# Kernel tuning notes

Measured on AMD Instinct MI355X. Metric: run time of the kernel, lower is better.

## Reference

```python
import jax, jax.numpy as jnp
import numpy as np

B, S, E, H = 2, 2048, 1024, 16
D = E // H  # head_dim = 64
SCALE = D ** -0.5
NEG = -1e9


def setup_inputs() -> dict:
    key = jax.random.key(0)
    ks = jax.random.split(key, 10)
    hidden_states = jax.random.normal(ks[0], (B, S, E), dtype=jnp.float32)
    # CLIP-style additive causal mask [B, 1, L, S]
    causal = jnp.where(jnp.tril(jnp.ones((S, S), dtype=bool)), 0.0, NEG).astype(jnp.float32)
    attn_mask = jnp.broadcast_to(causal, (B, 1, S, S))
    def lin(kw, kb):
        W = jax.random.normal(kw, (E, E), dtype=jnp.float32) * (E ** -0.5)
        b = jax.random.normal(kb, (E,), dtype=jnp.float32) * 0.02
        return W, b
    Wq, bq = lin(ks[1], ks[2])
    Wk, bk = lin(ks[3], ks[4])
    Wv, bv = lin(ks[5], ks[6])
    Wo, bo = lin(ks[7], ks[8])
    return {"hidden_states": hidden_states, "attn_mask": attn_mask,
            "Wq": Wq, "bq": bq, "Wk": Wk, "bk": bk,
            "Wv": Wv, "bv": bv, "Wo": Wo, "bo": bo}


def reference(hidden_states, attn_mask, Wq, bq, Wk, bk, Wv, bv, Wo, bo):
    b, L, e = hidden_states.shape
    # projections (nn.Linear: x @ W.T + b)
    def split_heads(x):
        return x.reshape(b, L, H, D).transpose(0, 2, 1, 3)  # [b,h,l,d]
    q = split_heads(hidden_states @ Wq.T + bq)
    k = split_heads(hidden_states @ Wk.T + bk)
    v = split_heads(hidden_states @ Wv.T + bv)
    # QK^T * scale + additive mask, softmax, AV (dropout_p = 0 in eval)
    scores = jnp.einsum('bhld,bhsd->bhls', q, k) * SCALE + attn_mask
    attn = jax.nn.softmax(scores, axis=-1)
    ctx = jnp.einsum('bhls,bhsd->bhld', attn, v)
    ctx = ctx.transpose(0, 2, 1, 3).reshape(b, L, e)
    return ctx @ Wo.T + bo
```

## Files before the change

kernel.cpp:

```cpp
#include <hip/hip_runtime.h>
#include <hip/hip_bf16.h>
#include <stdint.h>


typedef __hip_bfloat16 bf16;
typedef short bf16x8 __attribute__((ext_vector_type(8)));
typedef short bf16x4 __attribute__((ext_vector_type(4)));
typedef float f32x4 __attribute__((ext_vector_type(4)));

__device__ __forceinline__ f32x4 mfma16(bf16x8 a, bf16x8 b, f32x4 c) {
  return __builtin_amdgcn_mfma_f32_16x16x32_bf16(a, b, c, 0, 0, 0);
}

__device__ __forceinline__ f32x4 mfma_k16(bf16x4 a, bf16x4 b, f32x4 c) {
#if __has_builtin(__builtin_amdgcn_mfma_f32_16x16x16bf16_1k)
  return __builtin_amdgcn_mfma_f32_16x16x16bf16_1k(a, b, c, 0, 0, 0);
#else
  f32x4 d;
  asm volatile("v_mfma_f32_16x16x16_bf16 %0, %1, %2, %3\n\ts_nop 7\n\ts_nop 7"
               : "=v"(d)
               : "v"(a), "v"(b), "v"(c));
  return d;
#endif
}

__device__ __forceinline__ void async16(const void* g, void* l) {
  __builtin_amdgcn_global_load_lds((const __attribute__((address_space(1))) void*)g,
                                   (__attribute__((address_space(3))) void*)l, 16, 0, 0);
}

__global__ __launch_bounds__(256) void cvt_kernel(
    const float* __restrict__ hs, const float* __restrict__ Wq,
    const float* __restrict__ Wk, const float* __restrict__ Wv,
    const float* __restrict__ Wo, bf16* __restrict__ dst) {
  const size_t e = ((size_t)blockIdx.x * 256 + threadIdx.x) * 8;
  const float* src;
  size_t off;
  if (e < 4194304) {
    src = hs; off = e;
  } else {
    const size_t w = e - 4194304;
    const int wi = (int)(w >> 20);
    src = (wi == 0) ? Wq : (wi == 1) ? Wk : (wi == 2) ? Wv : Wo;
    off = w & 1048575;
  }
  const float4 a = *(const float4*)(src + off);
  const float4 b = *(const float4*)(src + off + 4);
  union { bf16 h[8]; uint4 u; } p;
  p.h[0] = __float2bfloat16(a.x); p.h[1] = __float2bfloat16(a.y);
  p.h[2] = __float2bfloat16(a.z); p.h[3] = __float2bfloat16(a.w);
  p.h[4] = __float2bfloat16(b.x); p.h[5] = __float2bfloat16(b.y);
  p.h[6] = __float2bfloat16(b.z); p.h[7] = __float2bfloat16(b.w);
  *(uint4*)(dst + e) = p.u;
}

__global__ __launch_bounds__(256, 3) void qkv_gemm(
    const bf16* __restrict__ X, const bf16* __restrict__ Wb,
    const float* __restrict__ bq, const float* __restrict__ bk,
    const float* __restrict__ bv, bf16* __restrict__ out) {
  constexpr int Kd = 1024;
  __shared__ bf16 sA[2][128 * 32];
  __shared__ bf16 sB[2][128 * 32];
  const int tid = threadIdx.x;
  const int wave = tid >> 6, lane = tid & 63;
  const int g = lane >> 4, ln = lane & 15;
  const int tM = blockIdx.y * 128, tN = blockIdx.x * 128;
  const int which = tN >> 10;
  const bf16* W = Wb + (size_t)which * 1048576;
  const float* bias = (which == 0) ? bq : (which == 1) ? bk : bv;
  const int tNl = tN & 1023;
  const float oscale = (which == 0) ? 0.18033688011112042f : 1.0f;
  const int wrow = (wave >> 1) * 64, wcol = (wave & 1) * 64;
  const f32x4 fz = {0.f, 0.f, 0.f, 0.f};

  f32x4 acc[4][4];
#pragma unroll
  for (int i = 0; i < 4; ++i)
#pragma unroll
    for (int j = 0; j < 4; ++j) acc[i][j] = fz;

  int srow[4], scol[4];
#pragma unroll
  for (int t = 0; t < 4; ++t) {
    const int d = tid + t * 256;
    srow[t] = (d >> 2) & 127;
    scol[t] = ((d >> 9) << 5) + ((d & 3) << 3);
  }

  for (int k0 = 0; k0 < Kd; k0 += 64) {
    __syncthreads();
#pragma unroll
    for (int t = 0; t < 4; ++t) {
      const int d = tid + t * 256;
      async16(X + (size_t)(tM + srow[t]) * Kd + k0 + scol[t], &sA[0][0] + d * 8);
      async16(W + (size_t)(tNl + srow[t]) * Kd + k0 + scol[t], &sB[0][0] + d * 8);
    }
    __syncthreads();
#pragma unroll
    for (int kk = 0; kk < 2; ++kk) {
      bf16x8 aF[4], bF[4];
#pragma unroll
      for (int i = 0; i < 4; ++i)
        aF[i] = *(const bf16x8*)(&sA[kk][0] + (wrow + i * 16 + ln) * 32 + g * 8);
#pragma unroll
      for (int j = 0; j < 4; ++j)
        bF[j] = *(const bf16x8*)(&sB[kk][0] + (wcol + j * 16 + ln) * 32 + g * 8);
#pragma unroll
      for (int i = 0; i < 4; ++i)
#pragma unroll
        for (int j = 0; j < 4; ++j) acc[i][j] = mfma16(aF[i], bF[j], acc[i][j]);
    }
  }

  bf16* outw = out + (size_t)which * 4194304;
#pragma unroll
  for (int j = 0; j < 4; ++j) {
    const int nl = tNl + wcol + j * 16 + ln;
    const float bvf = bias[nl];
    const int h = nl >> 6, d = nl & 63;
#pragma unroll
    for (int i = 0; i < 4; ++i) {
#pragma unroll
      for (int r = 0; r < 4; ++r) {
        const int m = tM + wrow + i * 16 + g * 4 + r;
        const int b = m >> 11, s = m & 2047;
        const float v = (acc[i][j][r] + bvf) * oscale;
        outw[(((size_t)(b * 16 + h) * 2048 + s) << 6) + d] = __float2bfloat16(v);
      }
    }
  }
}

__global__ __launch_bounds__(256, 4) void out_gemm(
    const bf16* __restrict__ X, const bf16* __restrict__ W,
    const float* __restrict__ bias, float* __restrict__ out) {
  constexpr int Kd = 1024;
  __shared__ bf16 sA[64 * 32];
  __shared__ bf16 sB[64 * 32];
  const int tid = threadIdx.x;
  const int wave = tid >> 6, lane = tid & 63;
  const int g = lane >> 4, ln = lane & 15;
  const int tM = blockIdx.y * 64, tN = blockIdx.x * 64;
  const f32x4 fz = {0.f, 0.f, 0.f, 0.f};

  f32x4 acc[4];
#pragma unroll
  for (int j = 0; j < 4; ++j) acc[j] = fz;

  const int srow = tid >> 2, scol = (tid & 3) << 3;
  for (int k0 = 0; k0 < Kd; k0 += 32) {
    __syncthreads();
    async16(X + (size_t)(tM + srow) * Kd + k0 + scol, sA + tid * 8);
    async16(W + (size_t)(tN + srow) * Kd + k0 + scol, sB + tid * 8);
    __syncthreads();
    const bf16x8 aF = *(const bf16x8*)(sA + (wave * 16 + ln) * 32 + g * 8);
    bf16x8 bF[4];
#pragma unroll
    for (int j = 0; j < 4; ++j)
      bF[j] = *(const bf16x8*)(sB + (j * 16 + ln) * 32 + g * 8);
#pragma unroll
    for (int j = 0; j < 4; ++j) acc[j] = mfma16(aF, bF[j], acc[j]);
  }

#pragma unroll
  for (int j = 0; j < 4; ++j) {
    const int n = tN + j * 16 + ln;
    const float bvf = bias[n];
#pragma unroll
    for (int r = 0; r < 4; ++r) {
      const int m = tM + wave * 16 + g * 4 + r;
      out[(size_t)m * 1024 + n] = acc[j][r] + bvf;
    }
  }
}

__global__ __launch_bounds__(256, 4) void attn_kernel(
    const bf16* __restrict__ Q, const bf16* __restrict__ K,
    const bf16* __restrict__ V, bf16* __restrict__ O) {
  constexpr int S = 2048, D = 64;
  __shared__ bf16 sK[64 * 72];
  __shared__ bf16 sVf[64 * 64];

  const int tid = threadIdx.x;
  const int w = tid >> 6, lane = tid & 63;
  const int g = lane >> 4, ln = lane & 15;
  const int px = blockIdx.x, py = blockIdx.y;
  const int bh = (px & 7) * 4 + (py & 3);
  const int qidx = (px >> 3) + 4 * (py >> 2);
  const int qt = 31 - qidx;
  const int b = bh >> 4, h = bh & 15;
  const f32x4 fz = {0.f, 0.f, 0.f, 0.f};

  const bf16* Qb = Q + (size_t)bh * S * D;
  const bf16* Kb = K + (size_t)bh * S * D;
  const bf16* Vb = V + (size_t)bh * S * D;

  const int kr0 = tid >> 3, kc0 = (tid & 7) << 3;
  int vsrc[2][4], vdst[2];
#pragma unroll
  for (int t = 0; t < 2; ++t) {
    const int c = tid + t * 256;
    const int u = c * 2;
    const int kbdb = u >> 6, vg = (u >> 4) & 3, l0 = u & 15;
    const int kb = kbdb >> 2, db = kbdb & 3;
#pragma unroll
    for (int i = 0; i < 4; ++i) vsrc[t][i] = (kb * 16 + vg * 4 + i) * 64 + db * 16 + l0;
    vdst[t] = c * 8;
  }

  bf16x8 qf[2];
#pragma unroll
  for (int kc = 0; kc < 2; ++kc)
    qf[kc] = *(const bf16x8*)(Qb + (size_t)(qt * 64 + w * 16 + ln) * D + kc * 32 + g * 8);

  f32x4 oacc[4];
#pragma unroll
  for (int db = 0; db < 4; ++db) oacc[db] = fz;
  f32x4 lacc = fz;
  const short onebf = (short)0x3F80;
  const bf16x4 onesf = {onebf, onebf, onebf, onebf};

  uint4 kreg0 = *(const uint4*)(Kb + (size_t)kr0 * D + kc0);
  uint4 kreg1 = *(const uint4*)(Kb + (size_t)(kr0 + 32) * D + kc0);
  uint32_t vreg[2][4];
#pragma unroll
  for (int t = 0; t < 2; ++t)
#pragma unroll
    for (int i = 0; i < 4; ++i) vreg[t][i] = *(const uint32_t*)(Vb + vsrc[t][i]);

  for (int kt = 0; kt <= qt; ++kt) {
    __syncthreads();
    *(uint4*)(sK + kr0 * 72 + kc0) = kreg0;
    *(uint4*)(sK + (kr0 + 32) * 72 + kc0) = kreg1;
#pragma unroll
    for (int t = 0; t < 2; ++t) {
      const uint32_t d0 = vreg[t][0], d1 = vreg[t][1], d2 = vreg[t][2], d3 = vreg[t][3];
      uint4 pk;
      pk.x = (d1 << 16) | (d0 & 0xffffu);
      pk.y = (d3 << 16) | (d2 & 0xffffu);
      pk.z = (d1 & 0xffff0000u) | (d0 >> 16);
      pk.w = (d3 & 0xffff0000u) | (d2 >> 16);
      *(uint4*)(sVf + vdst[t]) = pk;
    }
    __syncthreads();
    if (kt < qt) {
      const size_t nb = (size_t)(kt + 1) * 64;
      kreg0 = *(const uint4*)(Kb + (nb + kr0) * D + kc0);
      kreg1 = *(const uint4*)(Kb + (nb + kr0 + 32) * D + kc0);
#pragma unroll
      for (int t = 0; t < 2; ++t)
#pragma unroll
        for (int i = 0; i < 4; ++i)
          vreg[t][i] = *(const uint32_t*)(Vb + nb * D + vsrc[t][i]);
    }

    f32x4 sacc[4];
#pragma unroll
    for (int kb = 0; kb < 4; ++kb) sacc[kb] = fz;
#pragma unroll
    for (int kb = 0; kb < 4; ++kb) {
      const bf16x8 k0 = *(const bf16x8*)(sK + (kb * 16 + ln) * 72 + g * 8);
      const bf16x8 k1 = *(const bf16x8*)(sK + (kb * 16 + ln) * 72 + 32 + g * 8);
      sacc[kb] = mfma16(k0, qf[0], sacc[kb]);
      sacc[kb] = mfma16(k1, qf[1], sacc[kb]);
    }

    const bool diag = (kt == qt);
    const int qloc = w * 16 + ln;
    bf16x4 pa[4];
#pragma unroll
    for (int kb = 0; kb < 4; ++kb) {
      union { bf16 hh[4]; bf16x4 v; } pu;
#pragma unroll
      for (int r = 0; r < 4; ++r) {
        float pv = exp2f(sacc[kb][r]);
        if (diag && (kb * 16 + g * 4 + r > qloc)) pv = 0.f;
        pu.hh[r] = __float2bfloat16(pv);
      }
      pa[kb] = pu.v;
      lacc = mfma_k16(pa[kb], onesf, lacc);
    }

#pragma unroll
    for (int db = 0; db < 4; ++db) {
#pragma unroll
      for (int kb = 0; kb < 4; ++kb) {
        const bf16x4 vf =
            *(const bf16x4*)(sVf + ((kb * 4 + db) * 64 + g * 16 + ln) * 4);
        oacc[db] = mfma_k16(pa[kb], vf, oacc[db]);
      }
    }
  }

  float invl[4];
#pragma unroll
  for (int r = 0; r < 4; ++r) invl[r] = 1.0f / lacc[r];

#pragma unroll
  for (int db = 0; db < 4; ++db)
#pragma unroll
    for (int r = 0; r < 4; ++r) {
      const int row = qt * 64 + w * 16 + g * 4 + r;
      const int col = db * 16 + ln;
      O[(((size_t)(b * 2048 + row) * 16 + h) << 6) + col] =
          __float2bfloat16(oacc[db][r] * invl[r]);
    }
}

extern "C" void kernel_launch(void* const* d_in, const int* in_sizes, int n_in,
                              void* d_out, int out_size, void* d_ws, size_t ws_size,
                              hipStream_t stream) {
  const float* hs = (const float*)d_in[0];
  const float* Wq = (const float*)d_in[2];
  const float* bq = (const float*)d_in[3];
  const float* Wk = (const float*)d_in[4];
  const float* bk = (const float*)d_in[5];
  const float* Wv = (const float*)d_in[6];
  const float* bv = (const float*)d_in[7];
  const float* Wo = (const float*)d_in[8];
  const float* bo = (const float*)d_in[9];
  float* out = (float*)d_out;

  char* ws = (char*)d_ws;
  bf16* XW = (bf16*)ws;
  bf16* Xb = XW;
  bf16* W3b = XW + 4194304;
  bf16* Wob = XW + 7340032;
  bf16* Qw = (bf16*)(ws + (16u << 20));
  bf16* Kw = (bf16*)(ws + (24u << 20));
  bf16* Vw = (bf16*)(ws + (32u << 20));
  bf16* Cw = (bf16*)ws;

  const dim3 blk(256);
  cvt_kernel<<<4096, blk, 0, stream>>>(hs, Wq, Wk, Wv, Wo, XW);
  qkv_gemm<<<dim3(24, 32), blk, 0, stream>>>(Xb, W3b, bq, bk, bv, Qw);
  attn_kernel<<<dim3(32, 32), blk, 0, stream>>>(Qw, Kw, Vw, Cw);
  out_gemm<<<dim3(16, 64), blk, 0, stream>>>(Cw, Wob, bo, out);
}
```

Measured before the change: 200.7 us.

## Process 128 query rows per attention block with 512 threads sharing K/V tiles

The attention kernel now uses 512-thread blocks covering 128 query rows (8 waves), with half as many blocks. Each K/V tile staged in shared memory is reused by twice as many waves, and each thread loads one K row-chunk and one V chunk instead of two. Waves whose query rows lie entirely before the current key tile skip compute but still take part in the barriers. This adds idle waves on the diagonal tiles and heavier block-wide synchronisation in exchange for halving global K/V traffic.

```diff
diff --git a/kernel.cpp b/kernel.cpp
--- a/kernel.cpp
+++ b/kernel.cpp
@@ -174,7 +174,7 @@
   }
 }
 
-__global__ __launch_bounds__(256, 4) void attn_kernel(
+__global__ __launch_bounds__(512, 4) void attn_kernel(
     const bf16* __restrict__ Q, const bf16* __restrict__ K,
     const bf16* __restrict__ V, bf16* __restrict__ O) {
   constexpr int S = 2048, D = 64;
@@ -186,9 +186,12 @@
   const int g = lane >> 4, ln = lane & 15;
   const int px = blockIdx.x, py = blockIdx.y;
   const int bh = (px & 7) * 4 + (py & 3);
-  const int qidx = (px >> 3) + 4 * (py >> 2);
-  const int qt = 31 - qidx;
+  const int qp = (px >> 3) + 2 * (py >> 2);
+  const int t = 15 - qp;
   const int b = bh >> 4, h = bh & 15;
+  const int KT = 2 * t + 2;
+  const int qbase = t * 128 + w * 16;
+  const int dt = qbase >> 6;
   const f32x4 fz = {0.f, 0.f, 0.f, 0.f};
 
   const bf16* Qb = Q + (size_t)bh * S * D;
@@ -196,22 +199,20 @@
   const bf16* Vb = V + (size_t)bh * S * D;
 
   const int kr0 = tid >> 3, kc0 = (tid & 7) << 3;
-  int vsrc[2][4], vdst[2];
-#pragma unroll
-  for (int t = 0; t < 2; ++t) {
-    const int c = tid + t * 256;
-    const int u = c * 2;
+  int vsrc[4];
+  {
+    const int u = tid * 2;
     const int kbdb = u >> 6, vg = (u >> 4) & 3, l0 = u & 15;
     const int kb = kbdb >> 2, db = kbdb & 3;
 #pragma unroll
-    for (int i = 0; i < 4; ++i) vsrc[t][i] = (kb * 16 + vg * 4 + i) * 64 + db * 16 + l0;
-    vdst[t] = c * 8;
-  }
+    for (int i = 0; i < 4; ++i) vsrc[i] = (kb * 16 + vg * 4 + i) * 64 + db * 16 + l0;
+  }
+  const int vdst = tid * 8;
 
   bf16x8 qf[2];
 #pragma unroll
   for (int kc = 0; kc < 2; ++kc)
-    qf[kc] = *(const bf16x8*)(Qb + (size_t)(qt * 64 + w * 16 + ln) * D + kc * 32 + g * 8);
+    qf[kc] = *(const bf16x8*)(Qb + (size_t)(qbase + ln) * D + kc * 32 + g * 8);
 
   f32x4 oacc[4];
 #pragma unroll
@@ -220,75 +221,69 @@
   const short onebf = (short)0x3F80;
   const bf16x4 onesf = {onebf, onebf, onebf, onebf};
 
-  uint4 kreg0 = *(const uint4*)(Kb + (size_t)kr0 * D + kc0);
-  uint4 kreg1 = *(const uint4*)(Kb + (size_t)(kr0 + 32) * D + kc0);
-  uint32_t vreg[2][4];
-#pragma unroll
-  for (int t = 0; t < 2; ++t)
-#pragma unroll
-    for (int i = 0; i < 4; ++i) vreg[t][i] = *(const uint32_t*)(Vb + vsrc[t][i]);
-
-  for (int kt = 0; kt <= qt; ++kt) {
-    __syncthreads();
-    *(uint4*)(sK + kr0 * 72 + kc0) = kreg0;
-    *(uint4*)(sK + (kr0 + 32) * 72 + kc0) = kreg1;
-#pragma unroll
-    for (int t = 0; t < 2; ++t) {
-      const uint32_t d0 = vreg[t][0], d1 = vreg[t][1], d2 = vreg[t][2], d3 = vreg[t][3];
+  uint4 kreg = *(const uint4*)(Kb + (size_t)kr0 * D + kc0);
+  uint32_t vreg[4];
+#pragma unroll
+  for (int i = 0; i < 4; ++i) vreg[i] = *(const uint32_t*)(Vb + vsrc[i]);
+
+  for (int kt = 0; kt < KT; ++kt) {
+    __syncthreads();
+    *(uint4*)(sK + kr0 * 72 + kc0) = kreg;
+    {
+      const uint32_t d0 = vreg[0], d1 = vreg[1], d2 = vreg[2], d3 = vreg[3];
       uint4 pk;
       pk.x = (d1 << 16) | (d0 & 0xffffu);
       pk.y = (d3 << 16) | (d2 & 0xffffu);
       pk.z = (d1 & 0xffff0000u) | (d0 >> 16);
       pk.w = (d3 & 0xffff0000u) | (d2 >> 16);
-      *(uint4*)(sVf + vdst[t]) = pk;
-    }
-    __syncthreads();
-    if (kt < qt) {
+      *(uint4*)(sVf + vdst) = pk;
+    }
+    __syncthreads();
+    if (kt + 1 < KT) {
       const size_t nb = (size_t)(kt + 1) * 64;
-      kreg0 = *(const uint4*)(Kb + (nb + kr0) * D + kc0);
-      kreg1 = *(const uint4*)(Kb + (nb + kr0 + 32) * D + kc0);
-#pragma unroll
-      for (int t = 0; t < 2; ++t)
-#pragma unroll
-        for (int i = 0; i < 4; ++i)
-          vreg[t][i] = *(const uint32_t*)(Vb + nb * D + vsrc[t][i]);
-    }
-
-    f32x4 sacc[4];
-#pragma unroll
-    for (int kb = 0; kb < 4; ++kb) sacc[kb] = fz;
-#pragma unroll
-    for (int kb = 0; kb < 4; ++kb) {
-      const bf16x8 k0 = *(const bf16x8*)(sK + (kb * 16 + ln) * 72 + g * 8);
-      const bf16x8 k1 = *(const bf16x8*)(sK + (kb * 16 + ln) * 72 + 32 + g * 8);
-      sacc[kb] = mfma16(k0, qf[0], sacc[kb]);
-      sacc[kb] = mfma16(k1, qf[1], sacc[kb]);
-    }
-
-    const bool diag = (kt == qt);
-    const int qloc = w * 16 + ln;
-    bf16x4 pa[4];
-#pragma unroll
-    for (int kb = 0; kb < 4; ++kb) {
-      union { bf16 hh[4]; bf16x4 v; } pu;
-#pragma unroll
-      for (int r = 0; r < 4; ++r) {
-        float pv = exp2f(sacc[kb][r]);
-        if (diag && (kb * 16 + g * 4 + r > qloc)) pv = 0.f;
-        pu.hh[r] = __float2bfloat16(pv);
+      kreg = *(const uint4*)(Kb + (nb + kr0) * D + kc0);
+#pragma unroll
+      for (int i = 0; i < 4; ++i)
+        vreg[i] = *(const uint32_t*)(Vb + nb * D + vsrc[i]);
+    }
+
+    if (kt <= dt) {
+      f32x4 sacc[4];
+#pragma unroll
+      for (int kb = 0; kb < 4; ++kb) sacc[kb] = fz;
+#pragma unroll
+      for (int kb = 0; kb < 4; ++kb) {
+        const bf16x8 k0 = *(const bf16x8*)(sK + (kb * 16 + ln) * 72 + g * 8);
+        const bf16x8 k1 = *(const bf16x8*)(sK + (kb * 16 + ln) * 72 + 32 + g * 8);
+        sacc[kb] = mfma16(k0, qf[0], sacc[kb]);
+        sacc[kb] = mfma16(k1, qf[1], sacc[kb]);
       }
-      pa[kb] = pu.v;
-      lacc = mfma_k16(pa[kb], onesf, lacc);
-    }
-
-#pragma unroll
-    for (int db = 0; db < 4; ++db) {
+
+      const bool diag = (kt == dt);
+      const int qloc = (w & 3) * 16 + ln;
+      bf16x4 pa[4];
 #pragma unroll
       for (int kb = 0; kb < 4; ++kb) {
-        const bf16x4 vf =
-            *(const bf16x4*)(sVf + ((kb * 4 + db) * 64 + g * 16 + ln) * 4);
-        oacc[db] = mfma_k16(pa[kb], vf, oacc[db]);
+        union { bf16 hh[4]; bf16x4 v; } pu;
+#pragma unroll
+        for (int r = 0; r < 4; ++r) {
+          float pv = exp2f(sacc[kb][r]);
+          if (diag && (kb * 16 + g * 4 + r > qloc)) pv = 0.f;
+          pu.hh[r] = __float2bfloat16(pv);
+        }
+        pa[kb] = pu.v;
+        lacc = mfma_k16(pa[kb], onesf, lacc);
       }
+
+#pragma unroll
+      for (int db = 0; db < 4; ++db) {
+#pragma unroll
+        for (int kb = 0; kb < 4; ++kb) {
+          const bf16x4 vf =
+              *(const bf16x4*)(sVf + ((kb * 4 + db) * 64 + g * 16 + ln) * 4);
+          oacc[db] = mfma_k16(pa[kb], vf, oacc[db]);
+        }
+      }
     }
   }
 
@@ -300,7 +295,7 @@
   for (int db = 0; db < 4; ++db)
 #pragma unroll
     for (int r = 0; r < 4; ++r) {
-      const int row = qt * 64 + w * 16 + g * 4 + r;
+      const int row = qbase + g * 4 + r;
       const int col = db * 16 + ln;
       O[(((size_t)(b * 2048 + row) * 16 + h) << 6) + col] =
           __float2bfloat16(oacc[db][r] * invl[r]);
@@ -334,6 +329,6 @@
   const dim3 blk(256);
   cvt_kernel<<<4096, blk, 0, stream>>>(hs, Wq, Wk, Wv, Wo, XW);
   qkv_gemm<<<dim3(24, 32), blk, 0, stream>>>(Xb, W3b, bq, bk, bv, Qw);
-  attn_kernel<<<dim3(32, 32), blk, 0, stream>>>(Qw, Kw, Vw, Cw);
+  attn_kernel<<<dim3(16, 32), dim3(512), 0, stream>>>(Qw, Kw, Vw, Cw);
   out_gemm<<<dim3(16, 64), blk, 0, stream>>>(Cw, Wob, bo, out);
 }
```

New measurement: 207.2 us. +3.2%, slower.
